# Optimization experiments

Hardware: AMD Instinct MI355X
Metric: run time of the kernel (lower is better)

## Reference

```python
import jax, jax.numpy as jnp
import numpy as np

NUM_BBOX = 2
NUM_CLASSES = 20
NUM_GRID = 7
THR_CONF = 0.5
THR_NMS = 0.3
BATCH = 128


def setup_inputs() -> dict:
    key = jax.random.key(0)
    C = NUM_BBOX * 4 + NUM_BBOX + NUM_CLASSES  # 30
    p = jax.random.normal(key, (BATCH, NUM_GRID, NUM_GRID, C), dtype=jnp.float32)
    return {"p_yolo_ts4": p}


def _decode(p):
    B, S = p.shape[0], p.shape[1]
    sc = NUM_BBOX * 4
    conf = jax.nn.sigmoid(p[..., sc:sc + NUM_BBOX])          # [B,S,S,nb] objectness
    cls = jax.nn.sigmoid(p[..., sc + NUM_BBOX:])             # [B,S,S,nc]
    boxes = p[..., :sc].reshape(B, S, S, NUM_BBOX, 4)
    xy = jax.nn.sigmoid(boxes[..., :2])                      # cell-relative offsets
    col = jnp.arange(S, dtype=p.dtype)
    cx = (xy[..., 0] + col[None, None, :, None]) / NUM_GRID  # + col index (x)
    cy = (xy[..., 1] + col[None, :, None, None]) / NUM_GRID  # + row index (y)
    w, h = boxes[..., 2], boxes[..., 3]                      # raw wh, as in source
    ltrb = jnp.stack([cx - w / 2, cy - h / 2, cx + w / 2, cy + h / 2], axis=-1)
    labels = jnp.argmax(cls, axis=-1) + 1                    # [B,S,S]
    valid = conf > THR_CONF                                  # [B,S,S,nb]
    return ltrb, conf, labels, valid


def _pairwise_iou(b):
    lt = jnp.maximum(b[:, None, :2], b[None, :, :2])
    rb = jnp.minimum(b[:, None, 2:], b[None, :, 2:])
    wh = jnp.clip(rb - lt, 0.0)
    inter = wh[..., 0] * wh[..., 1]
    area = (b[:, 2] - b[:, 0]) * (b[:, 3] - b[:, 1])
    union = area[:, None] + area[None, :] - inter
    return inter / jnp.maximum(union, 1e-9)


def reference(p_yolo_ts4):
    p = p_yolo_ts4
    B, S = p.shape[0], p.shape[1]
    ltrb, conf, labels, valid = _decode(p)
    N = B * S * S * NUM_BBOX
    boxes = ltrb.reshape(N, 4)
    scores = conf.reshape(N)
    labs = jnp.broadcast_to(labels[..., None], (B, S, S, NUM_BBOX)).reshape(N)
    idsb = jnp.broadcast_to(jnp.arange(B)[:, None, None, None], (B, S, S, NUM_BBOX)).reshape(N)
    vmask = valid.reshape(N)
    # sort by score (invalid last); greedy NMS per (batch, label) group
    order = jnp.argsort(jnp.where(vmask, scores, -jnp.inf))[::-1]
    boxes_s = boxes[order]
    scores_s = scores[order]
    labs_s = labs[order]
    idsb_s = idsb[order]
    v_s = vmask[order]
    iou = _pairwise_iou(boxes_s)                              # [N,N]
    same = (idsb_s[:, None] == idsb_s[None, :]) & (labs_s[:, None] == labs_s[None, :])
    later = jnp.arange(N)[None, :] > jnp.arange(N)[:, None]
    sup_mat = (iou > THR_NMS) & same & later & v_s[None, :]

    def body(i, sup):
        keep_i = v_s[i] & jnp.logical_not(sup[i])
        return jnp.where(keep_i, sup | sup_mat[i], sup)

    sup = jax.lax.fori_loop(0, N, body, jnp.zeros((N,), dtype=bool))
    keep = v_s & jnp.logical_not(sup)
    # fixed-shape outputs in descending-score order; `keep` marks surviving boxes
    return idsb_s, boxes_s, labs_s, scores_s, keep
```

## Files before the change

kernel.cpp:

```cpp
#include <hip/hip_runtime.h>
#include <math.h>

#define NBATCH 128
#define S 7
#define CH 30
#define N 12544
#define PERB 98
#define CLEN 784
#define NCHUNK 16
#define THRNMS 0.3

__device__ __forceinline__ float sigf(float x) {
    float e = (float)exp(-(double)x);
    return 1.0f / (1.0f + e);
}

__device__ __forceinline__ float confraw(const float* __restrict__ p, int i) {
    return p[(i >> 1) * CH + 8 + (i & 1)];
}

__global__ __launch_bounds__(256) void k_rank(
    const float* __restrict__ p,
    unsigned int* __restrict__ vpart)
{
    __shared__ unsigned long long lk[CLEN];
    __shared__ unsigned int cnt_sh;
    const int tid = threadIdx.x;
    const int rb = blockIdx.x, ch = blockIdx.y;

    if (tid == 0) cnt_sh = 0u;
    __syncthreads();

    for (int u = tid; u < CLEN; u += 256) {
        int jg = ch * CLEN + u;
        float craw = confraw(p, jg);
        if (craw > 0.0f) {
            float sc = sigf(craw);
            if (sc > 0.5f) {
                unsigned int m = atomicAdd(&cnt_sh, 1u);
                lk[m] = ((unsigned long long)__float_as_uint(sc) << 32)
                        | (unsigned long long)(unsigned int)jg;
            }
        }
    }
    __syncthreads();
    const unsigned int len = cnt_sh;

    const int i = rb * 256 + tid;
    float crawi = confraw(p, i);
    bool validi = false;
    unsigned long long Ki = 0ull;
    if (crawi > 0.0f) {
        float sc = sigf(crawi);
        if (sc > 0.5f) {
            validi = true;
            Ki = ((unsigned long long)__float_as_uint(sc) << 32)
                 | (unsigned long long)(unsigned int)i;
        }
    }

    const unsigned int ui = (unsigned int)i;
    unsigned int cnt = 0;
    for (unsigned int u = 0; u < len; ++u) {
        unsigned long long K = lk[u];
        unsigned int c1 = (K > Ki) ? 1u : 0u;
        unsigned int c2 = ((unsigned int)K < ui) ? 1u : 0u;
        cnt += validi ? c1 : c2;
    }
    vpart[ch * N + i] = cnt;
}

__global__ __launch_bounds__(256) void k_finish(
    const float* __restrict__ p,
    const unsigned int* __restrict__ vpart,
    float* __restrict__ out)
{
    const int b   = blockIdx.x;
    const int tid = threadIdx.x;
    __shared__ int   lab49[49];
    __shared__ float bxa[PERB][4];
    __shared__ float sca[PERB];
    __shared__ unsigned long long Ka[PERB];
    __shared__ unsigned int posa[PERB];
    __shared__ int   srk[PERB];
    __shared__ float sbx[PERB][4];
    __shared__ int   slb[PERB], sup[PERB];
    __shared__ unsigned int kb_sh;

    if (tid == 0) kb_sh = 0u;

    if (tid < PERB) {
        int c = tid >> 1, half = tid & 1;
        const float* pc = p + (b * 49 + c) * CH;
        int cbase = 10 + half * 10;
        float best = sigf(pc[cbase]); int lab = half * 10;
        #pragma unroll
        for (int q = 1; q < 10; ++q) {
            float v = sigf(pc[cbase + q]);
            if (v > best) { best = v; lab = half * 10 + q; }
        }
        float obest = __shfl_xor(best, 1);
        int   olab  = __shfl_xor(lab, 1);
        float bestA = half ? obest : best;  int labA = half ? olab : lab;
        float bestB = half ? best  : obest; int labB = half ? lab  : olab;
        if (half == 0) lab49[c] = (bestB > bestA ? labB : labA) + 1;
    }

    if (tid < PERB) {
        int i = b * PERB + tid;
        int j = tid & 1, c = tid >> 1;
        const float* pc = p + (b * 49 + c) * CH;
        float tx = pc[j*4+0], ty = pc[j*4+1], tw = pc[j*4+2], th = pc[j*4+3];
        float craw = pc[8 + j];

        float sx = sigf(tx), sy = sigf(ty);
        int xg = c % S, yg = c / S;
        float cx = (sx + (float)xg) / 7.0f;
        float cy = (sy + (float)yg) / 7.0f;
        float hw = tw / 2.0f, hh = th / 2.0f;
        bxa[tid][0] = cx - hw; bxa[tid][1] = cy - hh;
        bxa[tid][2] = cx + hw; bxa[tid][3] = cy + hh;

        float sc = sigf(craw);
        sca[tid] = sc;
        bool valid = sc > 0.5f;
        Ka[tid] = valid ? (((unsigned long long)__float_as_uint(sc) << 32)
                           | (unsigned long long)(unsigned int)i)
                        : 0ull;

        unsigned int acc = 0;
        #pragma unroll
        for (int chn = 0; chn < NCHUNK; ++chn) acc += vpart[chn * N + i];
        posa[tid] = valid ? acc : (unsigned int)(N - 1 - i) + acc;
        if (valid) atomicAdd(&kb_sh, 1u);
    }
    __syncthreads();
    const int kb = (int)kb_sh;

    if (tid < PERB && Ka[tid] != 0ull) {
        unsigned long long Kt = Ka[tid];
        int rk = 0;
        for (int u = 0; u < PERB; ++u) rk += (Ka[u] > Kt) ? 1 : 0;
        srk[tid] = rk;
        sbx[rk][0] = bxa[tid][0]; sbx[rk][1] = bxa[tid][1];
        sbx[rk][2] = bxa[tid][2]; sbx[rk][3] = bxa[tid][3];
        slb[rk] = lab49[tid >> 1];
        sup[rk] = 0;
    }
    __syncthreads();

    for (int i = 0; i < kb; ++i) {
        __syncthreads();
        if (sup[i]) continue;
        float li = sbx[i][0], ti = sbx[i][1], ri = sbx[i][2], bi = sbx[i][3];
        float areai = (ri - li) * (bi - ti);
        int labi = slb[i];
        int jj = tid;
        if (jj > i && jj < kb && slb[jj] == labi) {
            float lj = sbx[jj][0], tj = sbx[jj][1], rj = sbx[jj][2], bj = sbx[jj][3];
            float lt0 = fmaxf(li, lj), lt1 = fmaxf(ti, tj);
            float rb0 = fminf(ri, rj), rb1 = fminf(bi, bj);
            float w = rb0 - lt0; if (w < 0.0f) w = 0.0f;
            float h = rb1 - lt1; if (h < 0.0f) h = 0.0f;
            float inter = w * h;
            float areaj = (rj - lj) * (bj - tj);
            float uni = areai + areaj - inter;
            double iou = (double)inter / fmax((double)uni, 1e-9);
            if (iou > THRNMS) sup[jj] = 1;
        }
    }
    __syncthreads();

    if (tid < PERB) {
        unsigned int pos = posa[tid];
        bool valid = Ka[tid] != 0ull;
        out[pos] = (float)b;
        ((float4*)(out + N))[pos] =
            make_float4(bxa[tid][0], bxa[tid][1], bxa[tid][2], bxa[tid][3]);
        out[5*N + pos] = (float)lab49[tid >> 1];
        out[6*N + pos] = sca[tid];
        out[7*N + pos] = (valid && !sup[srk[tid]]) ? 1.0f : 0.0f;
    }
}

extern "C" void kernel_launch(void* const* d_in, const int* in_sizes, int n_in,
                              void* d_out, int out_size, void* d_ws, size_t ws_size,
                              hipStream_t stream)
{
    const float* p = (const float*)d_in[0];
    float* out = (float*)d_out;
    unsigned int* vpart = (unsigned int*)d_ws;

    k_rank  <<<dim3(49, NCHUNK), dim3(256), 0, stream>>>(p, vpart);
    k_finish<<<dim3(NBATCH),     dim3(256), 0, stream>>>(p, vpart, out);
}
```

Baseline: 89.98 us.

## Precompute decoded keys in separate kernel and unify rank comparison into single key order

```diff
diff --git a/kernel.cpp b/kernel.cpp
--- a/kernel.cpp
+++ b/kernel.cpp
@@ -6,8 +6,8 @@
 #define CH 30
 #define N 12544
 #define PERB 98
+#define NCH 16
 #define CLEN 784
-#define NCHUNK 16
 #define THRNMS 0.3
 
 __device__ __forceinline__ float sigf(float x) {
@@ -15,72 +15,85 @@
     return 1.0f / (1.0f + e);
 }
 
-__device__ __forceinline__ float confraw(const float* __restrict__ p, int i) {
-    return p[(i >> 1) * CH + 8 + (i & 1)];
+__global__ __launch_bounds__(256) void k_decode(
+    const float* __restrict__ p,
+    unsigned long long* __restrict__ K,
+    float4* __restrict__ box4,
+    float* __restrict__ score,
+    int* __restrict__ meta)
+{
+    int i    = blockIdx.x * 256 + threadIdx.x;
+    int j    = i & 1;
+    int cell = i >> 1;
+    int x = cell % S, y = (cell / S) % S;
+    const float* pc = p + cell * CH;
+
+    float tx = pc[j*4+0], ty = pc[j*4+1], tw = pc[j*4+2], th = pc[j*4+3];
+    float craw = pc[8 + j];
+
+    int cbase = 10 + j * 10;
+    float best = sigf(pc[cbase]); int lab = j * 10;
+    #pragma unroll
+    for (int c = 1; c < 10; ++c) {
+        float v = sigf(pc[cbase + c]);
+        if (v > best) { best = v; lab = j * 10 + c; }
+    }
+    float obest = __shfl_xor(best, 1);
+    int   olab  = __shfl_xor(lab, 1);
+    float bestA = j ? obest : best;  int labA = j ? olab : lab;
+    float bestB = j ? best  : obest; int labB = j ? lab  : olab;
+    int label = (bestB > bestA ? labB : labA) + 1;
+
+    float sx = sigf(tx), sy = sigf(ty);
+    float cx = (sx + (float)x) / 7.0f;
+    float cy = (sy + (float)y) / 7.0f;
+    float hw = tw / 2.0f, hh = th / 2.0f;
+    float l = cx - hw, t = cy - hh, r = cx + hw, bt = cy + hh;
+
+    float sc = sigf(craw);
+    bool valid = sc > 0.5f;
+
+    K[i] = valid ? (((unsigned long long)__float_as_uint(sc) << 32)
+                    | (unsigned long long)(unsigned int)i)
+                 : (unsigned long long)(unsigned int)i;
+    box4[i]  = make_float4(l, t, r, bt);
+    score[i] = sc;
+    meta[i]  = label;
 }
 
 __global__ __launch_bounds__(256) void k_rank(
-    const float* __restrict__ p,
+    const unsigned long long* __restrict__ K,
     unsigned int* __restrict__ vpart)
 {
     __shared__ unsigned long long lk[CLEN];
-    __shared__ unsigned int cnt_sh;
     const int tid = threadIdx.x;
-    const int rb = blockIdx.x, ch = blockIdx.y;
+    const unsigned int base = blockIdx.y * CLEN;
 
-    if (tid == 0) cnt_sh = 0u;
+    for (int u = tid; u < CLEN; u += 256) lk[u] = K[base + u];
     __syncthreads();
 
-    for (int u = tid; u < CLEN; u += 256) {
-        int jg = ch * CLEN + u;
-        float craw = confraw(p, jg);
-        if (craw > 0.0f) {
-            float sc = sigf(craw);
-            if (sc > 0.5f) {
-                unsigned int m = atomicAdd(&cnt_sh, 1u);
-                lk[m] = ((unsigned long long)__float_as_uint(sc) << 32)
-                        | (unsigned long long)(unsigned int)jg;
-            }
-        }
-    }
-    __syncthreads();
-    const unsigned int len = cnt_sh;
-
-    const int i = rb * 256 + tid;
-    float crawi = confraw(p, i);
-    bool validi = false;
-    unsigned long long Ki = 0ull;
-    if (crawi > 0.0f) {
-        float sc = sigf(crawi);
-        if (sc > 0.5f) {
-            validi = true;
-            Ki = ((unsigned long long)__float_as_uint(sc) << 32)
-                 | (unsigned long long)(unsigned int)i;
-        }
-    }
-
-    const unsigned int ui = (unsigned int)i;
+    const unsigned int row = blockIdx.x * 256 + tid;
+    const unsigned long long Ki = K[row];
     unsigned int cnt = 0;
-    for (unsigned int u = 0; u < len; ++u) {
-        unsigned long long K = lk[u];
-        unsigned int c1 = (K > Ki) ? 1u : 0u;
-        unsigned int c2 = ((unsigned int)K < ui) ? 1u : 0u;
-        cnt += validi ? c1 : c2;
-    }
-    vpart[ch * N + i] = cnt;
+    #pragma unroll 8
+    for (int u = 0; u < CLEN; ++u)
+        cnt += (lk[u] > Ki) ? 1u : 0u;
+    vpart[blockIdx.y * N + row] = cnt;
 }
 
-__global__ __launch_bounds__(256) void k_finish(
-    const float* __restrict__ p,
+__global__ __launch_bounds__(128) void k_finish(
+    const unsigned long long* __restrict__ K,
+    const float4* __restrict__ box4,
+    const float* __restrict__ score,
+    const int* __restrict__ meta,
     const unsigned int* __restrict__ vpart,
     float* __restrict__ out)
 {
-    const int b   = blockIdx.x;
-    const int tid = threadIdx.x;
-    __shared__ int   lab49[49];
+    const int b = blockIdx.x, tid = threadIdx.x;
+    __shared__ unsigned long long Ka[PERB];
     __shared__ float bxa[PERB][4];
     __shared__ float sca[PERB];
-    __shared__ unsigned long long Ka[PERB];
+    __shared__ int   laba[PERB];
     __shared__ unsigned int posa[PERB];
     __shared__ int   srk[PERB];
     __shared__ float sbx[PERB][4];
@@ -88,63 +101,34 @@
     __shared__ unsigned int kb_sh;
 
     if (tid == 0) kb_sh = 0u;
-
-    if (tid < PERB) {
-        int c = tid >> 1, half = tid & 1;
-        const float* pc = p + (b * 49 + c) * CH;
-        int cbase = 10 + half * 10;
-        float best = sigf(pc[cbase]); int lab = half * 10;
-        #pragma unroll
-        for (int q = 1; q < 10; ++q) {
-            float v = sigf(pc[cbase + q]);
-            if (v > best) { best = v; lab = half * 10 + q; }
-        }
-        float obest = __shfl_xor(best, 1);
-        int   olab  = __shfl_xor(lab, 1);
-        float bestA = half ? obest : best;  int labA = half ? olab : lab;
-        float bestB = half ? best  : obest; int labB = half ? lab  : olab;
-        if (half == 0) lab49[c] = (bestB > bestA ? labB : labA) + 1;
-    }
+    __syncthreads();
 
     if (tid < PERB) {
         int i = b * PERB + tid;
-        int j = tid & 1, c = tid >> 1;
-        const float* pc = p + (b * 49 + c) * CH;
-        float tx = pc[j*4+0], ty = pc[j*4+1], tw = pc[j*4+2], th = pc[j*4+3];
-        float craw = pc[8 + j];
-
-        float sx = sigf(tx), sy = sigf(ty);
-        int xg = c % S, yg = c / S;
-        float cx = (sx + (float)xg) / 7.0f;
-        float cy = (sy + (float)yg) / 7.0f;
-        float hw = tw / 2.0f, hh = th / 2.0f;
-        bxa[tid][0] = cx - hw; bxa[tid][1] = cy - hh;
-        bxa[tid][2] = cx + hw; bxa[tid][3] = cy + hh;
-
-        float sc = sigf(craw);
-        sca[tid] = sc;
-        bool valid = sc > 0.5f;
-        Ka[tid] = valid ? (((unsigned long long)__float_as_uint(sc) << 32)
-                           | (unsigned long long)(unsigned int)i)
-                        : 0ull;
-
+        unsigned long long Kt = K[i];
+        Ka[tid] = Kt;
+        float4 v = box4[i];
+        bxa[tid][0] = v.x; bxa[tid][1] = v.y; bxa[tid][2] = v.z; bxa[tid][3] = v.w;
+        sca[tid]  = score[i];
+        laba[tid] = meta[i];
         unsigned int acc = 0;
         #pragma unroll
-        for (int chn = 0; chn < NCHUNK; ++chn) acc += vpart[chn * N + i];
-        posa[tid] = valid ? acc : (unsigned int)(N - 1 - i) + acc;
-        if (valid) atomicAdd(&kb_sh, 1u);
+        for (int ch = 0; ch < NCH; ++ch) acc += vpart[ch * N + i];
+        posa[tid] = acc;
+        if (Kt >> 32) atomicAdd(&kb_sh, 1u);
     }
     __syncthreads();
     const int kb = (int)kb_sh;
 
-    if (tid < PERB && Ka[tid] != 0ull) {
+    if (tid < PERB && (Ka[tid] >> 32)) {
         unsigned long long Kt = Ka[tid];
         int rk = 0;
-        for (int u = 0; u < PERB; ++u) rk += (Ka[u] > Kt) ? 1 : 0;
+        for (int u = 0; u < PERB; ++u)
+            rk += (Ka[u] > Kt) ? 1 : 0;
         srk[tid] = rk;
         sbx[rk][0] = bxa[tid][0]; sbx[rk][1] = bxa[tid][1];
         sbx[rk][2] = bxa[tid][2]; sbx[rk][3] = bxa[tid][3];
-        slb[rk] = lab49[tid >> 1];
+        slb[rk] = laba[tid];
         sup[rk] = 0;
     }
     __syncthreads();
@@ -173,11 +157,11 @@
 
     if (tid < PERB) {
         unsigned int pos = posa[tid];
-        bool valid = Ka[tid] != 0ull;
+        bool valid = (Ka[tid] >> 32) != 0ull;
         out[pos] = (float)b;
         ((float4*)(out + N))[pos] =
             make_float4(bxa[tid][0], bxa[tid][1], bxa[tid][2], bxa[tid][3]);
-        out[5*N + pos] = (float)lab49[tid >> 1];
+        out[5*N + pos] = (float)laba[tid];
         out[6*N + pos] = sca[tid];
         out[7*N + pos] = (valid && !sup[srk[tid]]) ? 1.0f : 0.0f;
     }
@@ -189,8 +173,15 @@
 {
     const float* p = (const float*)d_in[0];
     float* out = (float*)d_out;
-    unsigned int* vpart = (unsigned int*)d_ws;
 
-    k_rank  <<<dim3(49, NCHUNK), dim3(256), 0, stream>>>(p, vpart);
-    k_finish<<<dim3(NBATCH),     dim3(256), 0, stream>>>(p, vpart, out);
+    char* w = (char*)d_ws;
+    float4* box4        = (float4*)w;                     w += (size_t)N * 16;
+    unsigned long long* K = (unsigned long long*)w;       w += (size_t)N * 8;
+    float* score        = (float*)w;                      w += (size_t)N * 4;
+    int* meta           = (int*)w;                        w += (size_t)N * 4;
+    unsigned int* vpart = (unsigned int*)w;               w += (size_t)NCH * N * 4;
+
+    k_decode<<<dim3(N / 256),   dim3(256), 0, stream>>>(p, K, box4, score, meta);
+    k_rank  <<<dim3(49, NCH),   dim3(256), 0, stream>>>(K, vpart);
+    k_finish<<<dim3(NBATCH),    dim3(128), 0, stream>>>(K, box4, score, meta, vpart, out);
 }
```

New measurement: 89.31 us. Within noise of the previous version (-0.7%).
